# Optimization experiments

Measured on AMD Instinct MI355X. Metric: run time of the kernel, lower is better.

## Reference

```python
import jax, jax.numpy as jnp
import numpy as np
import math

D_MODEL = 512
N_HEADS = 8
D_FF = 2048
FACTOR = 5


def _layernorm(x, g, b, eps=1e-5):
    mu = jnp.mean(x, axis=-1, keepdims=True)
    var = jnp.mean((x - mu) ** 2, axis=-1, keepdims=True)
    return (x - mu) / jnp.sqrt(var + eps) * g + b


def setup_inputs() -> dict:
    key = jax.random.key(0)
    ks = jax.random.split(key, 12)
    B, L, D, F = 4, 2048, D_MODEL, D_FF
    sample_k = FACTOR * int(math.ceil(math.log(L)))  # 40
    x = jax.random.normal(ks[0], (B, L, D), dtype=jnp.float32)
    index_sample = jax.random.randint(ks[1], (L, sample_k), 0, L)
    s = 0.02
    inp = {
        'x': x,
        'index_sample': index_sample,
        'Wq': jax.random.normal(ks[2], (D, D), jnp.float32) * s, 'bq': jnp.zeros((D,), jnp.float32),
        'Wk': jax.random.normal(ks[3], (D, D), jnp.float32) * s, 'bk': jnp.zeros((D,), jnp.float32),
        'Wv': jax.random.normal(ks[4], (D, D), jnp.float32) * s, 'bv': jnp.zeros((D,), jnp.float32),
        'Wo': jax.random.normal(ks[5], (D, D), jnp.float32) * s, 'bo': jnp.zeros((D,), jnp.float32),
        'W1': jax.random.normal(ks[6], (F, D), jnp.float32) * s, 'b1': jnp.zeros((F,), jnp.float32),
        'W2': jax.random.normal(ks[7], (D, F), jnp.float32) * s, 'b2': jnp.zeros((D,), jnp.float32),
        'g1': jnp.ones((D,), jnp.float32), 'be1': jnp.zeros((D,), jnp.float32),
        'g2': jnp.ones((D,), jnp.float32), 'be2': jnp.zeros((D,), jnp.float32),
    }
    return inp


def _encoder_layer(x, index_sample, Wq, bq, Wk, bk, Wv, bv, Wo, bo, W1, b1, W2, b2, g1, be1, g2, be2):
    B, L, D = x.shape
    H = N_HEADS
    dk = D // H
    n_top = FACTOR * int(math.ceil(math.log(L)))  # 40; sparse branch since L*L > 40*40

    def split_heads(t):  # (B,L,D) -> (B,H,L,dk)
        return t.reshape(B, L, H, dk).transpose(0, 2, 1, 3)

    q = split_heads(x @ Wq.T + bq)
    k = split_heads(x @ Wk.T + bk)
    v = split_heads(x @ Wv.T + bv)

    # --- ProbSparse sampling: K_sample[b,h,i,j] = k[b,h,index_sample[i,j]] ---
    k_sample = k[:, :, index_sample, :]                      # (B,H,L,sample_k,dk)
    scores_sample = jnp.einsum('bhid,bhijd->bhij', q, k_sample)
    M = jnp.max(scores_sample, axis=-1) - jnp.sum(scores_sample, axis=-1) / L  # (B,H,L)
    _, top_idx = jax.lax.top_k(M, n_top)                     # (B,H,n_top)

    q_red = jnp.take_along_axis(q, top_idx[..., None], axis=2)  # (B,H,n_top,dk)
    scores_red = jnp.einsum('bhnd,bhkd->bhnk', q_red, k)        # NOTE: unscaled, as in source sparse branch

    bi = jnp.arange(B)[:, None, None]
    hi = jnp.arange(H)[None, :, None]
    scores = jnp.zeros((B, H, L, L), x.dtype).at[bi, hi, top_idx].set(scores_red)

    attn = jax.nn.softmax(scores, axis=-1)  # all-zero rows -> uniform (mean of V)
    ctx = jnp.einsum('bhqk,bhkd->bhqd', attn, v).transpose(0, 2, 1, 3).reshape(B, L, D)
    attn_out = ctx @ Wo.T + bo

    h1 = _layernorm(x + attn_out, g1, be1)
    ff = jax.nn.gelu(h1 @ W1.T + b1, approximate=False) @ W2.T + b2
    return _layernorm(h1 + ff, g2, be2)


def reference(x, index_sample, Wq, bq, Wk, bk, Wv, bv, Wo, bo, W1, b1, W2, b2, g1, be1, g2, be2):
    return _encoder_layer(x, index_sample, Wq, bq, Wk, bk, Wv, bv, Wo, bo,
                          W1, b1, W2, b2, g1, be1, g2, be2)
```

## Files before the change

### kernel.cpp

```cpp
#include <hip/hip_runtime.h>
#include <math.h>

#define L_SEQ   2048
#define DMODEL  512
#define NHEADS  8
#define DK      64
#define DFF     2048
#define BATCH   4
#define NTOP    40
#define MROWS   (BATCH*L_SEQ)
#define NCH     8
#define CHSZ    256
#define QPAD    48

typedef _Float16 f16;
typedef __attribute__((ext_vector_type(8))) _Float16 f16x8;
typedef __attribute__((ext_vector_type(8))) short    s16x8;
typedef __attribute__((ext_vector_type(4))) float    f32x4;

__device__ __forceinline__ ushort f2h_bits(float x) {
    f16 h = (f16)x;
    return __builtin_bit_cast(ushort, h);
}
__device__ __forceinline__ float h2f(ushort u) {
    return (float)__builtin_bit_cast(f16, u);
}

__device__ __forceinline__ float gelu_f(float v) {
    const float x = fabsf(v) * 0.70710678118654752f;
    const float t = 1.f / fmaf(0.3275911f, x, 1.f);
    float p = fmaf(1.061405429f, t, -1.453152027f);
    p = fmaf(p, t, 1.421413741f);
    p = fmaf(p, t, -0.284496736f);
    p = fmaf(p, t, 0.254829592f);
    p *= t;
    const float e = __expf(-x * x);
    const float erfv = copysignf(fmaf(-p, e, 1.f), v);
    return 0.5f * v * (1.f + erfv);
}

#define GLL16(gp, lp) \
    __builtin_amdgcn_global_load_lds((const __attribute__((address_space(1))) void*)(gp), \
                                     (__attribute__((address_space(3))) void*)(lp), 16, 0, 0)

__global__ __launch_bounds__(256)
void gemm_qkv(const ushort* __restrict__ xh, const ushort* __restrict__ xl,
              const ushort* __restrict__ wqh, const ushort* __restrict__ wql,
              const ushort* __restrict__ wkh, const ushort* __restrict__ wkl,
              const ushort* __restrict__ wvh,
              const float* __restrict__ bq, const float* __restrict__ bk,
              const float* __restrict__ bv,
              float* __restrict__ qo, float* __restrict__ kf,
              ushort* __restrict__ k16, ushort* __restrict__ vt16)
{
    __shared__ __align__(16) ushort sAh[128*32];
    __shared__ __align__(16) ushort sBh[128*32];
    __shared__ __align__(16) ushort sAl[128*32];
    __shared__ __align__(16) ushort sBl[128*32];

    const int z = blockIdx.z;
    const int m0 = blockIdx.y * 128;
    const int n0 = blockIdx.x * 128;
    const bool s3 = (z < 2);
    const ushort* Wh = (z == 0) ? wqh : (z == 1) ? wkh : wvh;
    const ushort* Wl = (z == 0) ? wql : wkl;
    const float*  bias = (z == 0) ? bq : (z == 1) ? bk : bv;
    const int K = DMODEL, N = DMODEL;

    const int tid  = threadIdx.x;
    const int wid  = tid >> 6, lane = tid & 63;
    const int wr   = (wid >> 1) * 64;
    const int wc   = (wid & 1) * 64;
    const int lr   = lane & 15;
    const int ko   = (lane >> 4) * 8;

    f32x4 acc[4][4];
#pragma unroll
    for (int i = 0; i < 4; ++i)
#pragma unroll
        for (int j = 0; j < 4; ++j) acc[i][j] = (f32x4){0.f, 0.f, 0.f, 0.f};

    const int sr = tid >> 2, sc = (tid & 3) * 8;
    const size_t gA = (size_t)(m0 + sr) * K + sc;
    const size_t gB = (size_t)(n0 + sr) * K + sc;
    const int l0 = tid * 8, l1 = tid * 8 + 2048;

    for (int k0 = 0; k0 < K; k0 += 32) {
        GLL16(xh + gA + k0,                sAh + l0);
        GLL16(xh + gA + (size_t)64*K + k0, sAh + l1);
        GLL16(Wh + gB + k0,                sBh + l0);
        GLL16(Wh + gB + (size_t)64*K + k0, sBh + l1);
        if (s3) {
            GLL16(xl + gA + k0,                sAl + l0);
            GLL16(xl + gA + (size_t)64*K + k0, sAl + l1);
            GLL16(Wl + gB + k0,                sBl + l0);
            GLL16(Wl + gB + (size_t)64*K + k0, sBl + l1);
        }
        __syncthreads();

        f16x8 ah[4], bh[4], al[4], bl[4];
#pragma unroll
        for (int i = 0; i < 4; ++i) {
            ah[i] = *(const f16x8*)&sAh[(wr + i*16 + lr) * 32 + ko];
            bh[i] = *(const f16x8*)&sBh[(wc + i*16 + lr) * 32 + ko];
            if (s3) {
                al[i] = *(const f16x8*)&sAl[(wr + i*16 + lr) * 32 + ko];
                bl[i] = *(const f16x8*)&sBl[(wc + i*16 + lr) * 32 + ko];
            }
        }
#pragma unroll
        for (int i = 0; i < 4; ++i)
#pragma unroll
            for (int j = 0; j < 4; ++j) {
                acc[i][j] = __builtin_amdgcn_mfma_f32_16x16x32_f16(ah[i], bh[j], acc[i][j], 0, 0, 0);
                if (s3) {
                    acc[i][j] = __builtin_amdgcn_mfma_f32_16x16x32_f16(ah[i], bl[j], acc[i][j], 0, 0, 0);
                    acc[i][j] = __builtin_amdgcn_mfma_f32_16x16x32_f16(al[i], bh[j], acc[i][j], 0, 0, 0);
                }
            }
        __syncthreads();
    }

    const int r0 = m0 + wr + (lane >> 4) * 4;
#pragma unroll
    for (int i = 0; i < 4; ++i)
#pragma unroll
        for (int j = 0; j < 4; ++j) {
            const int col = n0 + wc + j * 16 + lr;
            const float bb = bias[col];
#pragma unroll
            for (int qq = 0; qq < 4; ++qq) {
                const int row = r0 + i * 16 + qq;
                const float vv = acc[i][j][qq] + bb;
                if (z == 0) {
                    qo[(size_t)row * N + col] = vv;
                } else if (z == 1) {
                    kf [(size_t)row * N + col] = vv;
                    k16[(size_t)row * N + col] = f2h_bits(vv);
                } else {
                    vt16[((size_t)(row >> 11) * 512 + (col >> 6) * 64 + (col & 63)) * 2048 + (row & 2047)] = f2h_bits(vv);
                }
            }
        }
}

template<int ACT>
__global__ __launch_bounds__(256)
void gemm16(const ushort* __restrict__ Ah, const ushort* __restrict__ Wh,
            const float* __restrict__ bias, ushort* __restrict__ C16,
            int M, int N, int K)
{
    __shared__ __align__(16) ushort sAh[128*32];
    __shared__ __align__(16) ushort sBh[128*32];

    const int m0 = blockIdx.y * 128;
    const int n0 = blockIdx.x * 128;

    const int tid  = threadIdx.x;
    const int wid  = tid >> 6, lane = tid & 63;
    const int wr   = (wid >> 1) * 64;
    const int wc   = (wid & 1) * 64;
    const int lr   = lane & 15;
    const int ko   = (lane >> 4) * 8;

    f32x4 acc[4][4];
#pragma unroll
    for (int i = 0; i < 4; ++i)
#pragma unroll
        for (int j = 0; j < 4; ++j) acc[i][j] = (f32x4){0.f, 0.f, 0.f, 0.f};

    const int sr = tid >> 2, sc = (tid & 3) * 8;
    const size_t gA = (size_t)(m0 + sr) * K + sc;
    const size_t gB = (size_t)(n0 + sr) * K + sc;
    const int l0 = tid * 8, l1 = tid * 8 + 2048;

    for (int k0 = 0; k0 < K; k0 += 32) {
        GLL16(Ah + gA + k0,                sAh + l0);
        GLL16(Ah + gA + (size_t)64*K + k0, sAh + l1);
        GLL16(Wh + gB + k0,                sBh + l0);
        GLL16(Wh + gB + (size_t)64*K + k0, sBh + l1);
        __syncthreads();

        f16x8 ah[4], bh[4];
#pragma unroll
        for (int i = 0; i < 4; ++i) {
            ah[i] = *(const f16x8*)&sAh[(wr + i*16 + lr) * 32 + ko];
            bh[i] = *(const f16x8*)&sBh[(wc + i*16 + lr) * 32 + ko];
        }
#pragma unroll
        for (int i = 0; i < 4; ++i)
#pragma unroll
            for (int j = 0; j < 4; ++j)
                acc[i][j] = __builtin_amdgcn_mfma_f32_16x16x32_f16(ah[i], bh[j], acc[i][j], 0, 0, 0);
        __syncthreads();
    }

    const int r0 = m0 + wr + (lane >> 4) * 4;
#pragma unroll
    for (int i = 0; i < 4; ++i)
#pragma unroll
        for (int j = 0; j < 4; ++j) {
            const int col = n0 + wc + j * 16 + lr;
            const float bb = bias[col];
#pragma unroll
            for (int qq = 0; qq < 4; ++qq) {
                const int row = r0 + i * 16 + qq;
                float vv = acc[i][j][qq] + bb;
                if (ACT == 1) vv = gelu_f(vv);
                C16[(size_t)row * N + col] = f2h_bits(vv);
            }
        }
}

__global__ __launch_bounds__(256)
void gemm_sk(const ushort* __restrict__ Ah, const ushort* __restrict__ Wh,
             float* __restrict__ P0, float* __restrict__ P1, int K)
{
    __shared__ __align__(16) ushort sAh[128*32];
    __shared__ __align__(16) ushort sBh[128*32];

    const int z = blockIdx.z;
    const int m0 = blockIdx.y * 128;
    const int n0 = blockIdx.x * 128;
    const int khalf = K >> 1, kbase = z * khalf;
    const int N = DMODEL;
    float* __restrict__ P = z ? P1 : P0;

    const int tid  = threadIdx.x;
    const int wid  = tid >> 6, lane = tid & 63;
    const int wr   = (wid >> 1) * 64;
    const int wc   = (wid & 1) * 64;
    const int lr   = lane & 15;
    const int ko   = (lane >> 4) * 8;

    f32x4 acc[4][4];
#pragma unroll
    for (int i = 0; i < 4; ++i)
#pragma unroll
        for (int j = 0; j < 4; ++j) acc[i][j] = (f32x4){0.f, 0.f, 0.f, 0.f};

    const int sr = tid >> 2, sc = (tid & 3) * 8;
    const size_t gA = (size_t)(m0 + sr) * K + sc;
    const size_t gB = (size_t)(n0 + sr) * K + sc;
    const int l0 = tid * 8, l1 = tid * 8 + 2048;

    for (int k0 = kbase; k0 < kbase + khalf; k0 += 32) {
        GLL16(Ah + gA + k0,                sAh + l0);
        GLL16(Ah + gA + (size_t)64*K + k0, sAh + l1);
        GLL16(Wh + gB + k0,                sBh + l0);
        GLL16(Wh + gB + (size_t)64*K + k0, sBh + l1);
        __syncthreads();

        f16x8 ah[4], bh[4];
#pragma unroll
        for (int i = 0; i < 4; ++i) {
            ah[i] = *(const f16x8*)&sAh[(wr + i*16 + lr) * 32 + ko];
            bh[i] = *(const f16x8*)&sBh[(wc + i*16 + lr) * 32 + ko];
        }
#pragma unroll
        for (int i = 0; i < 4; ++i)
#pragma unroll
            for (int j = 0; j < 4; ++j)
                acc[i][j] = __builtin_amdgcn_mfma_f32_16x16x32_f16(ah[i], bh[j], acc[i][j], 0, 0, 0);
        __syncthreads();
    }

    const int r0 = m0 + wr + (lane >> 4) * 4;
#pragma unroll
    for (int i = 0; i < 4; ++i)
#pragma unroll
        for (int j = 0; j < 4; ++j) {
            const int col = n0 + wc + j * 16 + lr;
#pragma unroll
            for (int qq = 0; qq < 4; ++qq) {
                const int row = r0 + i * 16 + qq;
                P[(size_t)row * N + col] = acc[i][j][qq];
            }
        }
}

__device__ __forceinline__ void split8(const float* __restrict__ s,
                                       ushort* __restrict__ hi, ushort* __restrict__ lo)
{
    s16x8 h8, l8;
#pragma unroll
    for (int j = 0; j < 8; ++j) {
        float x = s[j];
        f16 hh = (f16)x;
        float r = x - (float)hh;
        f16 ll = (f16)r;
        h8[j] = (short)__builtin_bit_cast(ushort, hh);
        l8[j] = (short)__builtin_bit_cast(ushort, ll);
    }
    *(s16x8*)hi = h8;
    *(s16x8*)lo = l8;
}
__device__ __forceinline__ void cvt8(const float* __restrict__ s, ushort* __restrict__ d)
{
    s16x8 h8;
#pragma unroll
    for (int j = 0; j < 8; ++j) h8[j] = (short)f2h_bits(s[j]);
    *(s16x8*)d = h8;
}

__global__ __launch_bounds__(256)
void prep(const float* __restrict__ x,
          const float* __restrict__ Wq, const float* __restrict__ Wk,
          const float* __restrict__ Wv, const float* __restrict__ Wo,
          const float* __restrict__ W1, const float* __restrict__ W2,
          ushort* xh, ushort* xl,
          ushort* wqh, ushort* wql, ushort* wkh, ushort* wkl,
          ushort* wvh, ushort* woh, ushort* w1h, ushort* w2h)
{
    const int bid = blockIdx.x;
    if (bid < 2048) {
        const int t = bid * 256 + threadIdx.x;
        split8(x + (size_t)t * 8, xh + (size_t)t * 8, xl + (size_t)t * 8);
        return;
    }
    const int t = (bid - 2048) * 256 + threadIdx.x;
    const int e = t * 8;
    const int S = DMODEL * DMODEL;
    if      (e < S)           split8(Wq + e,           wqh + e,           wql + e);
    else if (e < 2*S)         split8(Wk + (e -   S),   wkh + (e -   S),   wkl + (e -   S));
    else if (e < 3*S)         cvt8  (Wv + (e - 2*S),   wvh + (e - 2*S));
    else if (e < 4*S)         cvt8  (Wo + (e - 3*S),   woh + (e - 3*S));
    else if (e < 4*S + DFF*DMODEL) cvt8(W1 + (e - 4*S), w1h + (e - 4*S));
    else                      cvt8  (W2 + (e - 4*S - DFF*DMODEL), w2h + (e - 4*S - DFF*DMODEL));
}

__global__ __launch_bounds__(256, 4)
void sample_scores(const float* __restrict__ q, const float* __restrict__ k,
                   const int* __restrict__ idxs, float* __restrict__ Mout)
{
    __shared__ float4 qs[4][128];

    const int bid = blockIdx.x;
    const int xcd = bid & 7;
    const int b   = xcd >> 1;
    const int chunk = (bid >> 3) * 2 + (xcd & 1);
    const int wid = threadIdx.x >> 6, lane = threadIdx.x & 63;
    const int i = chunk * 4 + wid;
    const int jsub = lane >> 3, c = lane & 7;

    {
        const float4* qrow = (const float4*)&q[((size_t)(b * L_SEQ + i)) * DMODEL];
        qs[wid][lane]      = qrow[lane];
        qs[wid][lane + 64] = qrow[lane + 64];
    }
    __syncthreads();

    const float4* kb = (const float4*)&k[(size_t)b * L_SEQ * DMODEL];

    float mx = -1e30f, sm = 0.f;
#pragma unroll
    for (int jb = 0; jb < 5; ++jb) {
        const int kidx = idxs[i * NTOP + jb * 8 + jsub];
        const float4* krow = kb + (size_t)kidx * (DMODEL / 4);
        float hacc[8];
#pragma unroll
        for (int u = 0; u < 8; ++u) hacc[u] = 0.f;
#pragma unroll
        for (int t = 0; t < 16; ++t) {
            const int p = t * 8 + c;
            const float4 kv = krow[p];
            const float4 qv = qs[wid][p];
            float d = 0.f;
            d = fmaf(qv.x, kv.x, d);
            d = fmaf(qv.y, kv.y, d);
            d = fmaf(qv.z, kv.z, d);
            d = fmaf(qv.w, kv.w, d);
            hacc[t >> 1] += d;
        }
#pragma unroll
        for (int s = 1; s < 8; s <<= 1)
#pragma unroll
            for (int u = 0; u < 8; ++u) hacc[u] += __shfl_xor(hacc[u], s);
        float sel = hacc[0];
#pragma unroll
        for (int u = 1; u < 8; ++u) sel = (c == u) ? hacc[u] : sel;
        mx = fmaxf(mx, sel);
        sm += sel;
    }
#pragma unroll
    for (int s = 8; s < 64; s <<= 1) {
        mx = fmaxf(mx, __shfl_xor(mx, s));
        sm += __shfl_xor(sm, s);
    }
    if (jsub == 0)
        Mout[((size_t)(b * NHEADS + c)) * L_SEQ + i] = mx - sm * (1.0f / (float)L_SEQ);
}

__global__ __launch_bounds__(256)
void topk40(const float* __restrict__ Mstat, int* __restrict__ top_idx)
{
    const int bh = blockIdx.x;
    __shared__ float vals[L_SEQ];
    __shared__ float wv[4];
    __shared__ int   wi[4];
    const int tid = threadIdx.x;
    const int lane = tid & 63, wid = tid >> 6;
    for (int t = tid; t < L_SEQ; t += 256) vals[t] = Mstat[(size_t)bh * L_SEQ + t];
    __syncthreads();

    for (int n = 0; n < NTOP; ++n) {
        float bv = -1e30f; int bi = L_SEQ;
#pragma unroll
        for (int r = 0; r < 8; ++r) {
            const int t = tid + r * 256;
            float vvv = vals[t];
            if (vvv > bv) { bv = vvv; bi = t; }
        }
#pragma unroll
        for (int s = 32; s > 0; s >>= 1) {
            float ov = __shfl_xor(bv, s); int oi = __shfl_xor(bi, s);
            if (ov > bv || (ov == bv && oi < bi)) { bv = ov; bi = oi; }
        }
        if (lane == 0) { wv[wid] = bv; wi[wid] = bi; }
        __syncthreads();
        if (tid == 0) {
            float fb = wv[0]; int fi = wi[0];
#pragma unroll
            for (int w = 1; w < 4; ++w)
                if (wv[w] > fb || (wv[w] == fb && wi[w] < fi)) { fb = wv[w]; fi = wi[w]; }
            top_idx[bh * NTOP + n] = fi;
            vals[fi] = -1e30f;
        }
        __syncthreads();
    }
}

__global__ __launch_bounds__(256)
void vmean_kernel(const ushort* __restrict__ vt, float* __restrict__ vmean)
{
    const int bh = blockIdx.x;
    const int wid = threadIdx.x >> 6, lane = threadIdx.x & 63;
#pragma unroll
    for (int dd = 0; dd < 16; ++dd) {
        const int d = wid * 16 + dd;
        const ushort* row = vt + ((size_t)bh * 64 + d) * 2048;
        float s = 0.f;
#pragma unroll
        for (int it = 0; it < 4; ++it) {
            s16x8 vv = *(const s16x8*)&row[it * 512 + lane * 8];
#pragma unroll
            for (int j = 0; j < 8; ++j) s += h2f((ushort)vv[j]);
        }
#pragma unroll
        for (int st = 1; st < 64; st <<= 1) s += __shfl_xor(s, st);
        if (lane == 0) vmean[bh * DK + d] = s * (1.0f / (float)L_SEQ);
    }
}

__global__ __launch_bounds__(256)
void fill_ctx(const float* __restrict__ vmean, ushort* __restrict__ ctx)
{
    const int t = blockIdx.x * 256 + threadIdx.x;
    const int e = t * 8;
    const int col = e & (DMODEL - 1);
    const int row = e >> 9;
    const int b = row >> 11;
    const int h = col >> 6, d = col & 63;
    const float* vm = &vmean[(b * 8 + h) * DK + d];
    s16x8 o;
#pragma unroll
    for (int j = 0; j < 8; ++j) o[j] = (short)f2h_bits(vm[j]);
    *(s16x8*)&ctx[e] = o;
}

__global__ __launch_bounds__(256, 1)
void attn_flash(const float* __restrict__ q, const ushort* __restrict__ k16,
                const ushort* __restrict__ vt16, const int* __restrict__ top_idx,
                float* __restrict__ part_o, float* __restrict__ part_ml)
{
    __shared__ __align__(16) ushort K_lds [CHSZ * 64];
    __shared__ __align__(16) ushort Vt_lds[64 * CHSZ];
    __shared__ __align__(16) ushort Q_lds [QPAD * 64];
    __shared__ __align__(16) ushort P_lds [QPAD * CHSZ];
    __shared__ float red_max[4][QPAD];
    __shared__ float red_sum[4][QPAD];

    const int bh = blockIdx.x >> 3, ch = blockIdx.x & 7;
    const int b = bh >> 3, h = bh & 7;
    const int tid = threadIdx.x;
    const int wid = tid >> 6, lane = tid & 63;
    const int lr = lane & 15, ks = lane >> 4;

    {
        const ushort* kbase = k16 + ((size_t)b * L_SEQ + ch * CHSZ) * DMODEL + h * DK;
#pragma unroll
        for (int it = 0; it < 8; ++it) {
            const int qi2 = wid * 8 + it;
            const int row = qi2 * 8 + (lane >> 3);
            const int g = (lane & 7) ^ (row & 7);
            GLL16(kbase + (size_t)row * DMODEL + g * 8, K_lds + qi2 * 512 + lane * 8);
        }
        const ushort* vtb = vt16 + ((size_t)bh * 64) * 2048 + ch * CHSZ;
#pragma unroll
        for (int it = 0; it < 8; ++it) {
            const int qi2 = wid * 8 + it;
            const int drow = qi2 * 2 + (lane >> 5);
            const int g = (lane & 31) ^ (drow & 7);
            GLL16(vtb + (size_t)drow * 2048 + g * 8, Vt_lds + qi2 * 512 + lane * 8);
        }
    }
    if (tid < QPAD * 4) {
        const int r = tid >> 2, part = tid & 3;
        s16x8 w0, w1;
        if (r < NTOP) {
            const int qi = top_idx[bh * NTOP + r];
            const float* qp = q + ((size_t)b * L_SEQ + qi) * DMODEL + h * DK + part * 16;
#pragma unroll
            for (int u = 0; u < 8; ++u) { w0[u] = (short)f2h_bits(qp[u]); w1[u] = (short)f2h_bits(qp[u + 8]); }
        } else {
#pragma unroll
            for (int u = 0; u < 8; ++u) { w0[u] = 0; w1[u] = 0; }
        }
        const int g0 = part * 2;
        *(s16x8*)((char*)Q_lds + r * 128 + (((g0    ) ^ (r & 7)) << 4)) = w0;
        *(s16x8*)((char*)Q_lds + r * 128 + (((g0 + 1) ^ (r & 7)) << 4)) = w1;
    }
    __syncthreads();

    f16x8 af[3][2], bf[4][2];
#pragma unroll
    for (int i = 0; i < 3; ++i)
#pragma unroll
        for (int kt = 0; kt < 2; ++kt) {
            const int row = i * 16 + lr;
            const int g = (kt * 4 + ks) ^ (row & 7);
            af[i][kt] = *(const f16x8*)((const char*)Q_lds + row * 128 + g * 16);
        }
#pragma unroll
    for (int j = 0; j < 4; ++j)
#pragma unroll
        for (int kt = 0; kt < 2; ++kt) {
            const int row = wid * 64 + j * 16 + lr;
            const int g = (kt * 4 + ks) ^ (row & 7);
            bf[j][kt] = *(const f16x8*)((const char*)K_lds + row * 128 + g * 16);
        }
    f32x4 acc[3][4];
#pragma unroll
    for (int i = 0; i < 3; ++i)
#pragma unroll
        for (int j = 0; j < 4; ++j) acc[i][j] = (f32x4){0.f, 0.f, 0.f, 0.f};
#pragma unroll
    for (int i = 0; i < 3; ++i)
#pragma unroll
        for (int j = 0; j < 4; ++j)
#pragma unroll
            for (int kt = 0; kt < 2; ++kt)
                acc[i][j] = __builtin_amdgcn_mfma_f32_16x16x32_f16(af[i][kt], bf[j][kt], acc[i][j], 0, 0, 0);

    float mrow[3][4];
#pragma unroll
    for (int i = 0; i < 3; ++i)
#pragma unroll
        for (int r = 0; r < 4; ++r) {
            float m = acc[i][0][r];
            m = fmaxf(m, acc[i][1][r]); m = fmaxf(m, acc[i][2][r]); m = fmaxf(m, acc[i][3][r]);
            mrow[i][r] = m;
        }
#pragma unroll
    for (int s = 1; s < 16; s <<= 1)
#pragma unroll
        for (int i = 0; i < 3; ++i)
#pragma unroll
            for (int r = 0; r < 4; ++r) mrow[i][r] = fmaxf(mrow[i][r], __shfl_xor(mrow[i][r], s));
    if (lr == 0)
#pragma unroll
        for (int i = 0; i < 3; ++i)
#pragma unroll
            for (int r = 0; r < 4; ++r) red_max[wid][i * 16 + ks * 4 + r] = mrow[i][r];
    __syncthreads();
    float mc[3][4];
#pragma unroll
    for (int i = 0; i < 3; ++i)
#pragma unroll
        for (int r = 0; r < 4; ++r) {
            const int row = i * 16 + ks * 4 + r;
            mc[i][r] = fmaxf(fmaxf(red_max[0][row], red_max[1][row]),
                             fmaxf(red_max[2][row], red_max[3][row]));
        }

    float srow[3][4];
#pragma unroll
    for (int i = 0; i < 3; ++i)
#pragma unroll
        for (int r = 0; r < 4; ++r) srow[i][r] = 0.f;
#pragma unroll
    for (int i = 0; i < 3; ++i)
#pragma unroll
        for (int j = 0; j < 4; ++j)
#pragma unroll
            for (int r = 0; r < 4; ++r) {
                const float p = expf(acc[i][j][r] - mc[i][r]);
                srow[i][r] += p;
                const int row = i * 16 + ks * 4 + r;
                const int cc = wid * 64 + j * 16 + lr;
                const int g = (cc >> 3) ^ (row & 7);
                *(ushort*)((char*)P_lds + row * 512 + g * 16 + (cc & 7) * 2) = f2h_bits(p);
            }
#pragma unroll
    for (int s = 1; s < 16; s <<= 1)
#pragma unroll
        for (int i = 0; i < 3; ++i)
#pragma unroll
            for (int r = 0; r < 4; ++r) srow[i][r] += __shfl_xor(srow[i][r], s);
    if (lr == 0)
#pragma unroll
        for (int i = 0; i < 3; ++i)
#pragma unroll
            for (int r = 0; r < 4; ++r) red_sum[wid][i * 16 + ks * 4 + r] = srow[i][r];
    __syncthreads();

    if (wid == 0 && lr == 0) {
#pragma unroll
        for (int i = 0; i < 3; ++i)
#pragma unroll
            for (int r = 0; r < 4; ++r) {
                const int row = i * 16 + ks * 4 + r;
                const float lc = red_sum[0][row] + red_sum[1][row] + red_sum[2][row] + red_sum[3][row];
                part_ml[(((size_t)bh * NCH + ch) * QPAD + row) * 2 + 0] = mc[i][r];
                part_ml[(((size_t)bh * NCH + ch) * QPAD + row) * 2 + 1] = lc;
            }
    }

    f32x4 acc2[3];
#pragma unroll
    for (int i = 0; i < 3; ++i) acc2[i] = (f32x4){0.f, 0.f, 0.f, 0.f};
#pragma unroll
    for (int kt = 0; kt < 8; ++kt) {
        f16x8 vb;
        {
            const int row = wid * 16 + lr;
            const int g = (kt * 4 + ks) ^ (row & 7);
            vb = *(const f16x8*)((const char*)Vt_lds + row * 512 + g * 16);
        }
#pragma unroll
        for (int i = 0; i < 3; ++i) {
            const int row = i * 16 + lr;
            const int g = (kt * 4 + ks) ^ (row & 7);
            const f16x8 pa = *(const f16x8*)((const char*)P_lds + row * 512 + g * 16);
            acc2[i] = __builtin_amdgcn_mfma_f32_16x16x32_f16(pa, vb, acc2[i], 0, 0, 0);
        }
    }
#pragma unroll
    for (int i = 0; i < 3; ++i)
#pragma unroll
        for (int r = 0; r < 4; ++r) {
            const int row = i * 16 + ks * 4 + r;
            const int d = wid * 16 + lr;
            part_o[((((size_t)bh * NCH + ch) * QPAD) + row) * 64 + d] = acc2[i][r];
        }
}

__global__ __launch_bounds__(256)
void attn_combine(const float* __restrict__ part_o, const float* __restrict__ part_ml,
                  const int* __restrict__ top_idx, ushort* __restrict__ ctx)
{
    const int bh = blockIdx.x;
    const int b = bh >> 3, h = bh & 7;
    const int d = threadIdx.x & 63, qg = threadIdx.x >> 6;
#pragma unroll
    for (int u = 0; u < 10; ++u) {
        const int qq = qg * 10 + u;
        float mv[NCH], lv[NCH];
        float m = -1e30f;
#pragma unroll
        for (int c = 0; c < NCH; ++c) {
            mv[c] = part_ml[(((size_t)bh * NCH + c) * QPAD + qq) * 2 + 0];
            lv[c] = part_ml[(((size_t)bh * NCH + c) * QPAD + qq) * 2 + 1];
            m = fmaxf(m, mv[c]);
        }
        float l = 0.f, o = 0.f;
#pragma unroll
        for (int c = 0; c < NCH; ++c) {
            const float e = expf(mv[c] - m);
            l += e * lv[c];
            o += e * part_o[((((size_t)bh * NCH + c) * QPAD) + qq) * 64 + d];
        }
        const int qi = top_idx[bh * NTOP + qq];
        ctx[((size_t)b * L_SEQ + qi) * DMODEL + h * DK + d] = f2h_bits(o / l);
    }
}

template<int W16>
__global__ __launch_bounds__(256)
void ln2(const float* __restrict__ a, const float* __restrict__ p0,
         const float* __restrict__ p1, const float* __restrict__ bias,
         const float* __restrict__ g, const float* __restrict__ be,
         float* __restrict__ out, ushort* __restrict__ out16)
{
    const int row = blockIdx.x; const int tid = threadIdx.x;
    const size_t base = (size_t)row * DMODEL;
    float x0 = a[base + tid]       + p0[base + tid]       + p1[base + tid]       + bias[tid];
    float x1 = a[base + 256 + tid] + p0[base + 256 + tid] + p1[base + 256 + tid] + bias[256 + tid];

    __shared__ float red[256];
    red[tid] = x0 + x1; __syncthreads();
    for (int st = 128; st > 0; st >>= 1) { if (tid < st) red[tid] += red[tid + st]; __syncthreads(); }
    const float mu = red[0] * (1.0f / (float)DMODEL);
    __syncthreads();

    const float d0 = x0 - mu, d1 = x1 - mu;
    red[tid] = d0 * d0 + d1 * d1; __syncthreads();
    for (int st = 128; st > 0; st >>= 1) { if (tid < st) red[tid] += red[tid + st]; __syncthreads(); }
    const float var = red[0] * (1.0f / (float)DMODEL);
    const float rstd = 1.0f / sqrtf(var + 1e-5f);

    const float y0 = d0 * rstd * g[tid]       + be[tid];
    const float y1 = d1 * rstd * g[256 + tid] + be[256 + tid];
    out[base + tid]       = y0;
    out[base + 256 + tid] = y1;
    if (W16) {
        out16[base + tid]       = f2h_bits(y0);
        out16[base + 256 + tid] = f2h_bits(y1);
    }
}

extern "C" void kernel_launch(void* const* d_in, const int* in_sizes, int n_in,
                              void* d_out, int out_size, void* d_ws, size_t ws_size,
                              hipStream_t stream)
{
    const float* x    = (const float*)d_in[0];
    const int*   idxs = (const int*)  d_in[1];
    const float* Wq = (const float*)d_in[2];  const float* bq = (const float*)d_in[3];
    const float* Wk = (const float*)d_in[4];  const float* bk = (const float*)d_in[5];
    const float* Wv = (const float*)d_in[6];  const float* bv = (const float*)d_in[7];
    const float* Wo = (const float*)d_in[8];  const float* bo = (const float*)d_in[9];
    const float* W1 = (const float*)d_in[10]; const float* b1 = (const float*)d_in[11];
    const float* W2 = (const float*)d_in[12]; const float* b2 = (const float*)d_in[13];
    const float* g1 = (const float*)d_in[14]; const float* be1= (const float*)d_in[15];
    const float* g2 = (const float*)d_in[16]; const float* be2= (const float*)d_in[17];

    const size_t MD = (size_t)MROWS * DMODEL;
    char* W = (char*)d_ws;
    ushort* xh    = (ushort*)(W);
    ushort* xl    = (ushort*)(W + 2*MD);
    float*  q     = (float*) (W + 4*MD);
    float*  k     = (float*) (W + 8*MD);
    ushort* k16   = (ushort*)(W + 12*MD);
    ushort* vt16  = (ushort*)(W + 14*MD);
    ushort* ctx16 = (ushort*)(W + 16*MD);
    float*  wo_p0 = (float*) (W);
    float*  wo_p1 = (float*) (W + 4*MD);
    float*  h1    = (float*) (W + 8*MD);
    ushort* h116  = (ushort*)(W + 12*MD);
    ushort* mid16 = (ushort*)(W);
    float*  w2_p0 = (float*) (W + 12*MD);
    float*  w2_p1 = (float*) (W + 16*MD);
    ushort* wqh   = (ushort*)(W + 20*MD);
    ushort* wql  = wqh + DMODEL*DMODEL;
    ushort* wkh  = wql + DMODEL*DMODEL;
    ushort* wkl  = wkh + DMODEL*DMODEL;
    ushort* wvh  = wkl + DMODEL*DMODEL;
    ushort* woh  = wvh + DMODEL*DMODEL;
    ushort* w1h  = woh + DMODEL*DMODEL;
    ushort* w2h  = w1h + DFF*DMODEL;
    float*  Mstat = (float*)(w2h + DMODEL*DFF);
    float*  vmean = Mstat + (size_t)BATCH * NHEADS * L_SEQ;
    int*    top_idx = (int*)(vmean + BATCH * NHEADS * DK);
    float*  part_o  = (float*)(top_idx + BATCH * NHEADS * NTOP);
    float*  part_ml = part_o + (size_t)BATCH * NHEADS * NCH * QPAD * 64;

    dim3 blk(256);

    prep<<<dim3(2048 + 1536), blk, 0, stream>>>(x, Wq, Wk, Wv, Wo, W1, W2,
                                                xh, xl, wqh, wql, wkh, wkl, wvh, woh, w1h, w2h);

    gemm_qkv<<<dim3(DMODEL/128, MROWS/128, 3), blk, 0, stream>>>(
        xh, xl, wqh, wql, wkh, wkl, wvh, bq, bk, bv, q, k, k16, vt16);

    sample_scores<<<dim3(2048), blk, 0, stream>>>(q, k, idxs, Mstat);
    topk40<<<dim3(BATCH*NHEADS), blk, 0, stream>>>(Mstat, top_idx);
    vmean_kernel<<<dim3(BATCH*NHEADS), blk, 0, stream>>>(vt16, vmean);
    fill_ctx<<<dim3(MD/2048), blk, 0, stream>>>(vmean, ctx16);
    attn_flash<<<dim3(BATCH*NHEADS*NCH), blk, 0, stream>>>(q, k16, vt16, top_idx, part_o, part_ml);
    attn_combine<<<dim3(BATCH*NHEADS), blk, 0, stream>>>(part_o, part_ml, top_idx, ctx16);

    gemm_sk<<<dim3(DMODEL/128, MROWS/128, 2), blk, 0, stream>>>(ctx16, woh, wo_p0, wo_p1, DMODEL);
    ln2<1><<<dim3(MROWS), blk, 0, stream>>>(x, wo_p0, wo_p1, bo, g1, be1, h1, h116);

    gemm16<1><<<dim3(DFF/128, MROWS/128), blk, 0, stream>>>(h116, w1h, b1, mid16, MROWS, DFF, DMODEL);
    gemm_sk<<<dim3(DMODEL/128, MROWS/128, 2), blk, 0, stream>>>(mid16, w2h, w2_p0, w2_p1, DFF);
    ln2<0><<<dim3(MROWS), blk, 0, stream>>>(h1, w2_p0, w2_p1, b2, g2, be2, (float*)d_out, nullptr);
}
```

Measured before the change: 285.6 us.

## Double-buffer LDS tiles in gemm16 and gemm_sk, use fast rcp in GELU

The FFN and split-K GEMMs now keep two LDS tile buffers, so the async global-to-LDS loads for the next K step are issued before the MFMA work on the current step, hiding load latency behind compute. One barrier per iteration remains. The GELU erf approximation swaps an IEEE divide for the hardware reciprocal instruction. LDS use per block doubles, which may lower occupancy, and the fast reciprocal slightly reduces precision.

Result: faster. 275.7 us (-3.5%).

```diff
diff --git a/kernel.cpp b/kernel.cpp
--- a/kernel.cpp
+++ b/kernel.cpp
@@ -28,7 +28,7 @@
 
 __device__ __forceinline__ float gelu_f(float v) {
     const float x = fabsf(v) * 0.70710678118654752f;
-    const float t = 1.f / fmaf(0.3275911f, x, 1.f);
+    const float t = __builtin_amdgcn_rcpf(fmaf(0.3275911f, x, 1.f));
     float p = fmaf(1.061405429f, t, -1.453152027f);
     p = fmaf(p, t, 1.421413741f);
     p = fmaf(p, t, -0.284496736f);
@@ -150,8 +150,8 @@
             const float* __restrict__ bias, ushort* __restrict__ C16,
             int M, int N, int K)
 {
-    __shared__ __align__(16) ushort sAh[128*32];
-    __shared__ __align__(16) ushort sBh[128*32];
+    __shared__ __align__(16) ushort sA[2][128*32];
+    __shared__ __align__(16) ushort sB[2][128*32];
 
     const int m0 = blockIdx.y * 128;
     const int n0 = blockIdx.x * 128;
@@ -174,18 +174,29 @@
     const size_t gB = (size_t)(n0 + sr) * K + sc;
     const int l0 = tid * 8, l1 = tid * 8 + 2048;
 
-    for (int k0 = 0; k0 < K; k0 += 32) {
-        GLL16(Ah + gA + k0,                sAh + l0);
-        GLL16(Ah + gA + (size_t)64*K + k0, sAh + l1);
-        GLL16(Wh + gB + k0,                sBh + l0);
-        GLL16(Wh + gB + (size_t)64*K + k0, sBh + l1);
-        __syncthreads();
-
+    GLL16(Ah + gA,                sA[0] + l0);
+    GLL16(Ah + gA + (size_t)64*K, sA[0] + l1);
+    GLL16(Wh + gB,                sB[0] + l0);
+    GLL16(Wh + gB + (size_t)64*K, sB[0] + l1);
+    __syncthreads();
+
+    const int nt = K >> 5;
+    int cur = 0;
+    for (int t = 0; t < nt; ++t) {
+        if (t + 1 < nt) {
+            const int k1 = (t + 1) << 5;
+            GLL16(Ah + gA + k1,                sA[cur ^ 1] + l0);
+            GLL16(Ah + gA + (size_t)64*K + k1, sA[cur ^ 1] + l1);
+            GLL16(Wh + gB + k1,                sB[cur ^ 1] + l0);
+            GLL16(Wh + gB + (size_t)64*K + k1, sB[cur ^ 1] + l1);
+        }
+        const ushort* A_ = sA[cur];
+        const ushort* B_ = sB[cur];
         f16x8 ah[4], bh[4];
 #pragma unroll
         for (int i = 0; i < 4; ++i) {
-            ah[i] = *(const f16x8*)&sAh[(wr + i*16 + lr) * 32 + ko];
-            bh[i] = *(const f16x8*)&sBh[(wc + i*16 + lr) * 32 + ko];
+            ah[i] = *(const f16x8*)&A_[(wr + i*16 + lr) * 32 + ko];
+            bh[i] = *(const f16x8*)&B_[(wc + i*16 + lr) * 32 + ko];
         }
 #pragma unroll
         for (int i = 0; i < 4; ++i)
@@ -193,6 +204,7 @@
             for (int j = 0; j < 4; ++j)
                 acc[i][j] = __builtin_amdgcn_mfma_f32_16x16x32_f16(ah[i], bh[j], acc[i][j], 0, 0, 0);
         __syncthreads();
+        cur ^= 1;
     }
 
     const int r0 = m0 + wr + (lane >> 4) * 4;
@@ -216,8 +228,8 @@
 void gemm_sk(const ushort* __restrict__ Ah, const ushort* __restrict__ Wh,
              float* __restrict__ P0, float* __restrict__ P1, int K)
 {
-    __shared__ __align__(16) ushort sAh[128*32];
-    __shared__ __align__(16) ushort sBh[128*32];
+    __shared__ __align__(16) ushort sA[2][128*32];
+    __shared__ __align__(16) ushort sB[2][128*32];
 
     const int z = blockIdx.z;
     const int m0 = blockIdx.y * 128;
@@ -244,18 +256,29 @@
     const size_t gB = (size_t)(n0 + sr) * K + sc;
     const int l0 = tid * 8, l1 = tid * 8 + 2048;
 
-    for (int k0 = kbase; k0 < kbase + khalf; k0 += 32) {
-        GLL16(Ah + gA + k0,                sAh + l0);
-        GLL16(Ah + gA + (size_t)64*K + k0, sAh + l1);
-        GLL16(Wh + gB + k0,                sBh + l0);
-        GLL16(Wh + gB + (size_t)64*K + k0, sBh + l1);
-        __syncthreads();
-
+    GLL16(Ah + gA + kbase,                sA[0] + l0);
+    GLL16(Ah + gA + (size_t)64*K + kbase, sA[0] + l1);
+    GLL16(Wh + gB + kbase,                sB[0] + l0);
+    GLL16(Wh + gB + (size_t)64*K + kbase, sB[0] + l1);
+    __syncthreads();
+
+    const int nt = khalf >> 5;
+    int cur = 0;
+    for (int t = 0; t < nt; ++t) {
+        if (t + 1 < nt) {
+            const int k1 = kbase + ((t + 1) << 5);
+            GLL16(Ah + gA + k1,                sA[cur ^ 1] + l0);
+            GLL16(Ah + gA + (size_t)64*K + k1, sA[cur ^ 1] + l1);
+            GLL16(Wh + gB + k1,                sB[cur ^ 1] + l0);
+            GLL16(Wh + gB + (size_t)64*K + k1, sB[cur ^ 1] + l1);
+        }
+        const ushort* A_ = sA[cur];
+        const ushort* B_ = sB[cur];
         f16x8 ah[4], bh[4];
 #pragma unroll
         for (int i = 0; i < 4; ++i) {
-            ah[i] = *(const f16x8*)&sAh[(wr + i*16 + lr) * 32 + ko];
-            bh[i] = *(const f16x8*)&sBh[(wc + i*16 + lr) * 32 + ko];
+            ah[i] = *(const f16x8*)&A_[(wr + i*16 + lr) * 32 + ko];
+            bh[i] = *(const f16x8*)&B_[(wc + i*16 + lr) * 32 + ko];
         }
 #pragma unroll
         for (int i = 0; i < 4; ++i)
@@ -263,6 +286,7 @@
             for (int j = 0; j < 4; ++j)
                 acc[i][j] = __builtin_amdgcn_mfma_f32_16x16x32_f16(ah[i], bh[j], acc[i][j], 0, 0, 0);
         __syncthreads();
+        cur ^= 1;
     }
 
     const int r0 = m0 + wr + (lane >> 4) * 4;
```
